# Kernel tuning notes

Measured on AMD Instinct MI355X. Metric: run time of the kernel, lower is better.

The kernel has to match this reference:

```python
import jax, jax.numpy as jnp
import numpy as np

B, S, E, H = 2, 2048, 1024, 16
D = E // H  # head_dim = 64


def setup_inputs() -> dict:
    key = jax.random.key(0)
    ks = jax.random.split(key, 14)
    inp = {
        "query": jax.random.normal(ks[0], (B, S, E), jnp.float32),
        "key": jax.random.normal(ks[1], (B, S, E), jnp.float32),
        "value": jax.random.normal(ks[2], (B, S, E), jnp.float32),
        "adj": jax.random.normal(ks[3], (S, S), jnp.float32),
        "mask": jax.random.randint(ks[4], (B, 1, S, S), 0, 2, jnp.int32),
    }
    sc = 1.0 / np.sqrt(E)
    inp["Wq"] = jax.random.normal(ks[5], (E, E), jnp.float32) * sc
    inp["bq"] = jax.random.normal(ks[6], (E,), jnp.float32) * sc
    inp["Wk"] = jax.random.normal(ks[7], (E, E), jnp.float32) * sc
    inp["bk"] = jax.random.normal(ks[8], (E,), jnp.float32) * sc
    inp["Wv"] = jax.random.normal(ks[9], (E, E), jnp.float32) * sc
    inp["bv"] = jax.random.normal(ks[10], (E,), jnp.float32) * sc
    inp["Wo"] = jax.random.normal(ks[11], (E, E), jnp.float32) * sc
    inp["bo"] = jax.random.normal(ks[12], (E,), jnp.float32) * sc
    return inp


def reference(query, key, value, adj, mask, Wq, bq, Wk, bk, Wv, bv, Wo, bo):
    b, s, _ = query.shape
    # projections, split into heads: [B,S,E] -> [B,H,S,D]
    def heads(x, W, bias):
        y = jnp.einsum("bse,ef->bsf", x, W.T) + bias
        return y.reshape(b, s, H, D).transpose(0, 2, 1, 3)

    Q = heads(query, Wq, bq)
    K = heads(key, Wk, bk)
    V = heads(value, Wv, bv)

    # scores: [B,H,S,S], scaled by sqrt(head_dim), plus adjacency bias
    scores = jnp.einsum("bhqd,bhkd->bhqk", Q, K) / jnp.sqrt(jnp.float32(D))
    scores = scores + adj[None, None, :, :]
    scores = jnp.where(mask == 0, jnp.float32(-jnp.inf), scores)

    weights = jax.nn.softmax(scores, axis=-1)
    out = jnp.einsum("bhqk,bhkd->bhqd", weights, V)
    out = out.transpose(0, 2, 1, 3).reshape(b, s, E)
    return jnp.einsum("bse,ef->bsf", out, Wo.T) + bo
```

## Files before the change

kernel.cpp:

```cpp
#include <hip/hip_runtime.h>


typedef unsigned short ushort_t;
typedef __attribute__((ext_vector_type(8))) short bf16x8;
typedef __attribute__((ext_vector_type(4))) float floatx4;
typedef __attribute__((ext_vector_type(2))) unsigned int uintx2;

#define NB 2
#define NS 2048
#define NE 1024
#define NH 16
#define ND 64
#define LOG2E 1.44269504f

__device__ __forceinline__ unsigned short f2bf(float f) {
  unsigned int u = __float_as_uint(f);
  return (unsigned short)((u + 0x7fffu + ((u >> 16) & 1u)) >> 16);
}
__device__ __forceinline__ float bf2f(unsigned short h) {
  return __uint_as_float(((unsigned int)h) << 16);
}

__device__ __forceinline__ void gload_lds16(const void* g, void* l) {
  __builtin_amdgcn_global_load_lds(
      (const __attribute__((address_space(1))) unsigned int*)g,
      (__attribute__((address_space(3))) unsigned int*)l, 16, 0, 0);
}

__device__ __forceinline__ float fexp2(float x) {
#if __has_builtin(__builtin_amdgcn_exp2f)
  return __builtin_amdgcn_exp2f(x);
#else
  return exp2f(x);
#endif
}

__device__ __forceinline__ unsigned int cvtpk_bf16(float lo, float hi) {
  unsigned int r;
  asm("v_cvt_pk_bf16_f32 %0, %1, %2" : "=v"(r) : "v"(lo), "v"(hi));
  return r;
}

__device__ __forceinline__ void pl32swap(unsigned int& a, unsigned int& b) {
#if __has_builtin(__builtin_amdgcn_permlane32_swap)
  uintx2 r = __builtin_amdgcn_permlane32_swap(a, b, false, false);
  a = r[0]; b = r[1];
#else
  asm("v_permlane32_swap_b32 %0, %1" : "+v"(a), "+v"(b));
#endif
}
__device__ __forceinline__ void pl16swap(unsigned int& a, unsigned int& b) {
#if __has_builtin(__builtin_amdgcn_permlane16_swap)
  uintx2 r = __builtin_amdgcn_permlane16_swap(a, b, false, false);
  a = r[0]; b = r[1];
#else
  asm("v_permlane16_swap_b32 %0, %1" : "+v"(a), "+v"(b));
#endif
}

__global__ __launch_bounds__(256) void convert_kernel(
    const float* __restrict__ q, const float* __restrict__ k, const float* __restrict__ v,
    const float* __restrict__ wq, const float* __restrict__ wk,
    const float* __restrict__ wv, const float* __restrict__ wo,
    const float* __restrict__ adj, const int* __restrict__ mask,
    ushort_t* __restrict__ qb, ushort_t* __restrict__ kb, ushort_t* __restrict__ vb,
    ushort_t* __restrict__ wqb, ushort_t* __restrict__ wkb,
    ushort_t* __restrict__ wvb, ushort_t* __restrict__ wob,
    ushort_t* __restrict__ bias)
{
  const long U1 = (long)NB * NS * NE / 8;
  const long U2 = (long)NE * NE / 8;
  long idx = (long)blockIdx.x * 256 + threadIdx.x;
  const float* src;
  ushort_t* dst;
  if (idx < U1) { src = q; dst = qb; }
  else if ((idx -= U1) < U1) { src = k; dst = kb; }
  else if ((idx -= U1) < U1) { src = v; dst = vb; }
  else if ((idx -= U1) < U2) { src = wq; dst = wqb; }
  else if ((idx -= U2) < U2) { src = wk; dst = wkb; }
  else if ((idx -= U2) < U2) { src = wv; dst = wvb; }
  else if ((idx -= U2) < U2) { src = wo; dst = wob; }
  else {
    idx -= U2;
    long flat = idx * 8;
    long rem = flat & ((1L << 22) - 1);
    const float4* a4 = (const float4*)(adj + rem);
    const int4* m4 = (const int4*)(mask + flat);
    float4 a0 = a4[0], a1 = a4[1];
    int4 m0 = m4[0], m1 = m4[1];
    const float NEGV = -1e30f;
    union { ushort_t us[8]; uint4 v4; } o;
    o.us[0] = f2bf((m0.x ? a0.x : NEGV) * LOG2E);
    o.us[1] = f2bf((m0.y ? a0.y : NEGV) * LOG2E);
    o.us[2] = f2bf((m0.z ? a0.z : NEGV) * LOG2E);
    o.us[3] = f2bf((m0.w ? a0.w : NEGV) * LOG2E);
    o.us[4] = f2bf((m1.x ? a1.x : NEGV) * LOG2E);
    o.us[5] = f2bf((m1.y ? a1.y : NEGV) * LOG2E);
    o.us[6] = f2bf((m1.z ? a1.z : NEGV) * LOG2E);
    o.us[7] = f2bf((m1.w ? a1.w : NEGV) * LOG2E);
    ((uint4*)bias)[idx] = o.v4;
    return;
  }
  const float4* s4 = (const float4*)src;
  float4 a0 = s4[idx * 2], a1 = s4[idx * 2 + 1];
  union { ushort_t us[8]; uint4 v4; } o;
  o.us[0] = f2bf(a0.x); o.us[1] = f2bf(a0.y); o.us[2] = f2bf(a0.z); o.us[3] = f2bf(a0.w);
  o.us[4] = f2bf(a1.x); o.us[5] = f2bf(a1.y); o.us[6] = f2bf(a1.z); o.us[7] = f2bf(a1.w);
  ((uint4*)dst)[idx] = o.v4;
}

__global__ __launch_bounds__(256) void qkv_kernel(
    const ushort_t* __restrict__ xq, const ushort_t* __restrict__ xk, const ushort_t* __restrict__ xv,
    const ushort_t* __restrict__ wqb, const ushort_t* __restrict__ wkb, const ushort_t* __restrict__ wvb,
    const float* __restrict__ bq, const float* __restrict__ bk, const float* __restrict__ bvv,
    ushort_t* __restrict__ Qh, ushort_t* __restrict__ Kh, ushort_t* __restrict__ Vt)
{
  __shared__ __align__(16) ushort_t As[128 * 32];
  __shared__ __align__(16) ushort_t Bs[128 * 32];

  int z = blockIdx.z;
  const ushort_t* X = (z == 0) ? xq : (z == 1) ? xk : xv;
  const ushort_t* W = (z == 0) ? wqb : (z == 1) ? wkb : wvb;
  const float* bias = (z == 0) ? bq : (z == 1) ? bk : bvv;

  int t = threadIdx.x;
  int lane = t & 63, w = t >> 6;
  int quad = lane >> 4, l16 = lane & 15;
  int wr = w >> 1, wc = w & 1;
  int m0 = blockIdx.y * 128, f0 = blockIdx.x * 128;

  floatx4 acc[4][4] = {};

  int arow = t >> 2, apart = t & 3;
  const ushort_t* Xg = X + (long)(m0 + arow) * NE + apart * 8;
  const ushort_t* Wg = W + (long)(f0 + arow) * NE + apart * 8;
  ushort_t* As_t = As + t * 8;
  ushort_t* Bs_t = Bs + t * 8;

  for (int k0 = 0; k0 < NE; k0 += 32) {
    __syncthreads();
    gload_lds16(Xg + k0, As_t);
    gload_lds16(Xg + k0 + 64 * NE, As_t + 64 * 32);
    gload_lds16(Wg + k0, Bs_t);
    gload_lds16(Wg + k0 + 64 * NE, Bs_t + 64 * 32);
    __syncthreads();
    bf16x8 af[4], bf[4];
#pragma unroll
    for (int i = 0; i < 4; i++)
      af[i] = *(const bf16x8*)(As + (wr * 64 + i * 16 + l16) * 32 + quad * 8);
#pragma unroll
    for (int j = 0; j < 4; j++)
      bf[j] = *(const bf16x8*)(Bs + (wc * 64 + j * 16 + l16) * 32 + quad * 8);
#pragma unroll
    for (int i = 0; i < 4; i++)
#pragma unroll
      for (int j = 0; j < 4; j++)
        acc[i][j] = __builtin_amdgcn_mfma_f32_16x16x32_bf16(af[i], bf[j], acc[i][j], 0, 0, 0);
  }

  ushort_t* Out = (z == 0) ? Qh : (z == 1) ? Kh : Vt;
  bool isV = (z == 2);
#pragma unroll
  for (int j = 0; j < 4; j++) {
    int f = f0 + wc * 64 + j * 16 + l16;
    float bval = bias[f];
    int h = f >> 6, d = f & 63;
#pragma unroll
    for (int i = 0; i < 4; i++) {
      int mbase = m0 + wr * 64 + i * 16 + quad * 4;
#pragma unroll
      for (int r = 0; r < 4; r++) {
        int m = mbase + r;
        int b = m >> 11, s = m & 2047;
        float y = acc[i][j][r] + bval;
        long off;
        if (!isV) off = ((long)(b * NH + h) * NS + s) * ND + d;
        else      off = ((long)(b * NH + h) * ND + d) * NS + s;
        Out[off] = f2bf(y);
      }
    }
  }
}

__global__ __launch_bounds__(256, 2) void attn_kernel(
    const ushort_t* __restrict__ Qh, const ushort_t* __restrict__ Kh,
    const ushort_t* __restrict__ Vt, const ushort_t* __restrict__ bias,
    ushort_t* __restrict__ aout)
{
  __shared__ __align__(16) ushort_t Qs[128 * 64];
  __shared__ __align__(16) ushort_t Ks[2][32 * 64];
  __shared__ __align__(16) ushort_t Vts[2][64 * 32];

  int t = threadIdx.x, lane = t & 63, w = t >> 6;
  int quad = lane >> 4, l16 = lane & 15;
  int orig = blockIdx.y * 16 + blockIdx.x;
  int wg = ((orig & 7) << 6) | (orig >> 3);
  int qt = wg & 15, bh = wg >> 4;
  int bb = bh >> 4, h = bh & 15;
  int q0 = qt * 128;

  const ushort_t* Qg = Qh + ((long)bh * NS + q0) * ND;
#pragma unroll
  for (int c = 0; c < 4; c++) {
    int idx = c * 256 + t;
    gload_lds16(Qg + (long)(idx >> 3) * ND + (idx & 7) * 8, Qs + idx * 8);
  }

  const ushort_t* Kg = Kh + (long)bh * NS * ND;
  const ushort_t* Vg = Vt + (long)bh * ND * NS;
  int krow = t >> 3;
  int kc = (t & 7) ^ (krow & 7);
  int vsr = t >> 3;
  int vc = (t & 7) ^ (vsr & 7);
  int vrow = vsr * 2 + (vc >> 2);
  int vpart = vc & 3;
  const ushort_t* Kgp = Kg + (long)krow * ND + kc * 8;
  const ushort_t* Vgp = Vg + (long)vrow * NS + vpart * 8;

  gload_lds16(Kgp, &Ks[0][t * 8]);
  gload_lds16(Vgp, &Vts[0][t * 8]);

  const ushort_t* bg0 = bias + (long)bb * NS * NS
                      + (long)(q0 + w * 32 + l16) * NS + quad * 4;
  const ushort_t* bg1 = bg0 + 16 * NS;
  uintx2 bc[2][2];
  bc[0][0] = *(const uintx2*)bg0;
  bc[0][1] = *(const uintx2*)(bg0 + 16);
  bc[1][0] = *(const uintx2*)bg1;
  bc[1][1] = *(const uintx2*)(bg1 + 16);

  __syncthreads();

  bf16x8 aq[2][2];
#pragma unroll
  for (int m = 0; m < 2; m++)
#pragma unroll
    for (int kd = 0; kd < 2; kd++)
      aq[m][kd] = *(const bf16x8*)(Qs + (w * 32 + m * 16 + l16) * 64 + kd * 32 + quad * 8);

  floatx4 acc[2][4] = {};
  float lsum[2] = {0.f, 0.f};

  const int ks_x = l16 & 7;
  const int vs_c = (((l16 & 1) * 4 + quad) ^ (l16 >> 1)) * 8;

#pragma unroll 2
  for (int kt = 0; kt < NS / 32; kt++) {
    int cur = kt & 1;
    __syncthreads();
    if (kt < NS / 32 - 1) {
      gload_lds16(Kgp + (long)(kt + 1) * (32 * ND), &Ks[cur ^ 1][t * 8]);
      gload_lds16(Vgp + (kt + 1) * 32, &Vts[cur ^ 1][t * 8]);
    }
    uintx2 bn[2][2];
#pragma unroll
    for (int m = 0; m < 2; m++) { bn[m][0] = bc[m][0]; bn[m][1] = bc[m][1]; }
    if (kt < NS / 32 - 1) {
      bn[0][0] = *(const uintx2*)(bg0 + (kt + 1) * 32);
      bn[0][1] = *(const uintx2*)(bg0 + (kt + 1) * 32 + 16);
      bn[1][0] = *(const uintx2*)(bg1 + (kt + 1) * 32);
      bn[1][1] = *(const uintx2*)(bg1 + (kt + 1) * 32 + 16);
    }

    const ushort_t* Kb = Ks[cur];
    const ushort_t* Vb = Vts[cur];
    bf16x8 bk[2][2], bv[4];
#pragma unroll
    for (int jk = 0; jk < 2; jk++)
#pragma unroll
      for (int kd = 0; kd < 2; kd++)
        bk[jk][kd] = *(const bf16x8*)(Kb + (jk * 16 + l16) * 64
                                         + ((kd * 4 + quad) ^ ks_x) * 8);
#pragma unroll
    for (int j = 0; j < 4; j++)
      bv[j] = *(const bf16x8*)(Vb + (j * 8 + (l16 >> 1)) * 64 + vs_c);

#pragma unroll
    for (int m = 0; m < 2; m++) {
      floatx4 sc[2] = {};
#pragma unroll
      for (int jk = 0; jk < 2; jk++)
#pragma unroll
        for (int kd = 0; kd < 2; kd++)
          sc[jk] = __builtin_amdgcn_mfma_f32_16x16x32_bf16(bk[jk][kd], aq[m][kd], sc[jk], 0, 0, 0);

      float p[2][4];
#pragma unroll
      for (int jk = 0; jk < 2; jk++) {
        unsigned int d0 = bc[m][jk][0], d1 = bc[m][jk][1];
        float b0 = __uint_as_float(d0 << 16);
        float b1 = __uint_as_float(d0 & 0xffff0000u);
        float b2 = __uint_as_float(d1 << 16);
        float b3 = __uint_as_float(d1 & 0xffff0000u);
        p[jk][0] = fexp2(fmaf(sc[jk][0], 0.125f * LOG2E, b0));
        p[jk][1] = fexp2(fmaf(sc[jk][1], 0.125f * LOG2E, b1));
        p[jk][2] = fexp2(fmaf(sc[jk][2], 0.125f * LOG2E, b2));
        p[jk][3] = fexp2(fmaf(sc[jk][3], 0.125f * LOG2E, b3));
      }
      lsum[m] += ((p[0][0] + p[0][1]) + (p[0][2] + p[0][3]))
               + ((p[1][0] + p[1][1]) + (p[1][2] + p[1][3]));

      unsigned int A0 = cvtpk_bf16(p[0][0], p[0][1]);
      unsigned int A1 = cvtpk_bf16(p[0][2], p[0][3]);
      unsigned int B0 = cvtpk_bf16(p[1][0], p[1][1]);
      unsigned int B1 = cvtpk_bf16(p[1][2], p[1][3]);
      pl32swap(A0, B0); pl16swap(A0, B0);
      pl32swap(A1, B1); pl16swap(A1, B1);
      union { unsigned int u[4]; bf16x8 v8; } pf;
      pf.u[0] = A0; pf.u[1] = A1; pf.u[2] = B0; pf.u[3] = B1;
#pragma unroll
      for (int j = 0; j < 4; j++)
        acc[m][j] = __builtin_amdgcn_mfma_f32_16x16x32_bf16(pf.v8, bv[j], acc[m][j], 0, 0, 0);
    }
#pragma unroll
    for (int m = 0; m < 2; m++) { bc[m][0] = bn[m][0]; bc[m][1] = bn[m][1]; }
  }

#pragma unroll
  for (int m = 0; m < 2; m++) {
    float s = lsum[m];
    s += __shfl_xor(s, 16);
    s += __shfl_xor(s, 32);
    lsum[m] = s;
  }

  ushort_t* og = aout + (long)bb * NS * NE + h * ND;
#pragma unroll
  for (int m = 0; m < 2; m++)
#pragma unroll
    for (int r = 0; r < 4; r++) {
      float inv = 1.0f / __shfl(lsum[m], quad * 4 + r);
      int qg = q0 + w * 32 + m * 16 + quad * 4 + r;
#pragma unroll
      for (int j = 0; j < 4; j++)
        og[(long)qg * NE + j * 16 + l16] = f2bf(acc[m][j][r] * inv);
    }
}

__global__ __launch_bounds__(256) void oproj_kernel(
    const ushort_t* __restrict__ A, const ushort_t* __restrict__ Wob,
    const float* __restrict__ bo, float* __restrict__ out)
{
  __shared__ __align__(16) ushort_t As[128 * 32];
  __shared__ __align__(16) ushort_t Bs[64 * 32];

  int t = threadIdx.x;
  int lane = t & 63, w = t >> 6;
  int quad = lane >> 4, l16 = lane & 15;
  int wr = w >> 1, wc = w & 1;
  int m0 = blockIdx.y * 128, f0 = blockIdx.x * 64;

  floatx4 acc[4][2] = {};
  int arow = t >> 2, apart = t & 3;
  const ushort_t* Xg = A + (long)(m0 + arow) * NE + apart * 8;
  const ushort_t* Wg = Wob + (long)(f0 + arow) * NE + apart * 8;
  ushort_t* As_t = As + t * 8;
  ushort_t* Bs_t = Bs + t * 8;
  bool bstage = (arow < 64);

  for (int k0 = 0; k0 < NE; k0 += 32) {
    __syncthreads();
    gload_lds16(Xg + k0, As_t);
    gload_lds16(Xg + k0 + 64 * NE, As_t + 64 * 32);
    if (bstage) gload_lds16(Wg + k0, Bs_t);
    __syncthreads();
    bf16x8 af[4], bf[2];
#pragma unroll
    for (int i = 0; i < 4; i++)
      af[i] = *(const bf16x8*)(As + (wr * 64 + i * 16 + l16) * 32 + quad * 8);
#pragma unroll
    for (int j = 0; j < 2; j++)
      bf[j] = *(const bf16x8*)(Bs + (wc * 32 + j * 16 + l16) * 32 + quad * 8);
#pragma unroll
    for (int i = 0; i < 4; i++)
#pragma unroll
      for (int j = 0; j < 2; j++)
        acc[i][j] = __builtin_amdgcn_mfma_f32_16x16x32_bf16(af[i], bf[j], acc[i][j], 0, 0, 0);
  }

#pragma unroll
  for (int j = 0; j < 2; j++) {
    int f = f0 + wc * 32 + j * 16 + l16;
    float bval = bo[f];
#pragma unroll
    for (int i = 0; i < 4; i++) {
      int mbase = m0 + wr * 64 + i * 16 + quad * 4;
#pragma unroll
      for (int r = 0; r < 4; r++) {
        int m = mbase + r;
        out[(long)m * NE + f] = acc[i][j][r] + bval;
      }
    }
  }
}

extern "C" void kernel_launch(void* const* d_in, const int* in_sizes, int n_in,
                              void* d_out, int out_size, void* d_ws, size_t ws_size,
                              hipStream_t stream) {
  const float* query = (const float*)d_in[0];
  const float* key   = (const float*)d_in[1];
  const float* value = (const float*)d_in[2];
  const float* adj   = (const float*)d_in[3];
  const int*   mask  = (const int*)d_in[4];
  const float* Wq = (const float*)d_in[5];
  const float* bq = (const float*)d_in[6];
  const float* Wk = (const float*)d_in[7];
  const float* bk = (const float*)d_in[8];
  const float* Wv = (const float*)d_in[9];
  const float* bv = (const float*)d_in[10];
  const float* Wo = (const float*)d_in[11];
  const float* bo = (const float*)d_in[12];
  float* out = (float*)d_out;

  char* ws = (char*)d_ws;
  const size_t MB = 1ull << 20;
  ushort_t* qb   = (ushort_t*)(ws + 0 * MB);
  ushort_t* kb   = (ushort_t*)(ws + 8 * MB);
  ushort_t* vb   = (ushort_t*)(ws + 16 * MB);
  ushort_t* wqb  = (ushort_t*)(ws + 24 * MB);
  ushort_t* wkb  = (ushort_t*)(ws + 26 * MB);
  ushort_t* wvb  = (ushort_t*)(ws + 28 * MB);
  ushort_t* wob  = (ushort_t*)(ws + 30 * MB);
  ushort_t* Qh   = (ushort_t*)(ws + 32 * MB);
  ushort_t* Kh   = (ushort_t*)(ws + 40 * MB);
  ushort_t* Vt   = (ushort_t*)(ws + 48 * MB);
  ushort_t* aout = (ushort_t*)(ws + 56 * MB);
  ushort_t* bias = (ushort_t*)(ws + 64 * MB);

  convert_kernel<<<12288, 256, 0, stream>>>(query, key, value, Wq, Wk, Wv, Wo,
                                            adj, mask, qb, kb, vb, wqb, wkb, wvb, wob, bias);
  qkv_kernel<<<dim3(8, 32, 3), 256, 0, stream>>>(qb, kb, vb, wqb, wkb, wvb,
                                                 bq, bk, bv, Qh, Kh, Vt);
  attn_kernel<<<dim3(16, 32), 256, 0, stream>>>(Qh, Kh, Vt, bias, aout);
  oproj_kernel<<<dim3(16, 32), 256, 0, stream>>>(aout, wob, bo, out);
}
```

Before: 313.3 us.

## Triple-buffer GEMM loads and split attention keys across two waves per block

The QKV and output-projection GEMMs move to a three-stage LDS ring with explicit vmcnt waits and a single barrier per iteration, so global loads can overlap MFMA work. The attention kernel is restructured into 128-thread blocks of 64 queries. Each of its two waves handles half of the key range with its own private K/V double buffer and no block barriers inside the loop. The two partial outputs and row sums are then merged through LDS. This adds more register pressure (4x4 accumulators), hand-tuned waitcnt counts that could break correctness if they are wrong, and a reduction epilogue.

New measurement: 328.7 us. +4.9%, slower.

```diff
diff --git a/kernel.cpp b/kernel.cpp
--- a/kernel.cpp
+++ b/kernel.cpp
@@ -25,6 +25,13 @@
   __builtin_amdgcn_global_load_lds(
       (const __attribute__((address_space(1))) unsigned int*)g,
       (__attribute__((address_space(3))) unsigned int*)l, 16, 0, 0);
+}
+
+__device__ __forceinline__ uintx2 gload8(const void* p) {
+  uintx2 r;
+  asm volatile("global_load_dwordx2 %0, %1, off"
+               : "=v"(r) : "v"(p) : "memory");
+  return r;
 }
 
 __device__ __forceinline__ float fexp2(float x) {
@@ -115,8 +122,8 @@
     const float* __restrict__ bq, const float* __restrict__ bk, const float* __restrict__ bvv,
     ushort_t* __restrict__ Qh, ushort_t* __restrict__ Kh, ushort_t* __restrict__ Vt)
 {
-  __shared__ __align__(16) ushort_t As[128 * 32];
-  __shared__ __align__(16) ushort_t Bs[128 * 32];
+  __shared__ __align__(16) ushort_t As[3][128 * 32];
+  __shared__ __align__(16) ushort_t Bs[3][128 * 32];
 
   int z = blockIdx.z;
   const ushort_t* X = (z == 0) ? xq : (z == 1) ? xk : xv;
@@ -129,34 +136,45 @@
   int wr = w >> 1, wc = w & 1;
   int m0 = blockIdx.y * 128, f0 = blockIdx.x * 128;
 
-  floatx4 acc[4][4] = {};
-
   int arow = t >> 2, apart = t & 3;
   const ushort_t* Xg = X + (long)(m0 + arow) * NE + apart * 8;
   const ushort_t* Wg = W + (long)(f0 + arow) * NE + apart * 8;
-  ushort_t* As_t = As + t * 8;
-  ushort_t* Bs_t = Bs + t * 8;
-
-  for (int k0 = 0; k0 < NE; k0 += 32) {
-    __syncthreads();
-    gload_lds16(Xg + k0, As_t);
-    gload_lds16(Xg + k0 + 64 * NE, As_t + 64 * 32);
-    gload_lds16(Wg + k0, Bs_t);
-    gload_lds16(Wg + k0 + 64 * NE, Bs_t + 64 * 32);
-    __syncthreads();
+
+  auto STAGE = [&](int kk, int buf) {
+    int k0 = kk * 32;
+    gload_lds16(Xg + k0, &As[buf][t * 8]);
+    gload_lds16(Xg + k0 + 64 * NE, &As[buf][64 * 32 + t * 8]);
+    gload_lds16(Wg + k0, &Bs[buf][t * 8]);
+    gload_lds16(Wg + k0 + 64 * NE, &Bs[buf][64 * 32 + t * 8]);
+  };
+  STAGE(0, 0);
+  STAGE(1, 1);
+
+  floatx4 acc[4][4] = {};
+  int b = 0;
+  for (int k = 0; k < 32; ++k) {
+    asm volatile("s_waitcnt vmcnt(4) lgkmcnt(0)" ::: "memory");
+    __builtin_amdgcn_s_barrier();
+    __builtin_amdgcn_sched_barrier(0);
+    int nb = (b == 0) ? 2 : b - 1;
+    STAGE((k + 2) & 31, nb);
+    const ushort_t* Ab = As[b];
+    const ushort_t* Bb = Bs[b];
     bf16x8 af[4], bf[4];
 #pragma unroll
     for (int i = 0; i < 4; i++)
-      af[i] = *(const bf16x8*)(As + (wr * 64 + i * 16 + l16) * 32 + quad * 8);
-#pragma unroll
-    for (int j = 0; j < 4; j++)
-      bf[j] = *(const bf16x8*)(Bs + (wc * 64 + j * 16 + l16) * 32 + quad * 8);
+      af[i] = *(const bf16x8*)(Ab + (wr * 64 + i * 16 + l16) * 32 + quad * 8);
+#pragma unroll
+    for (int j = 0; j < 4; j++)
+      bf[j] = *(const bf16x8*)(Bb + (wc * 64 + j * 16 + l16) * 32 + quad * 8);
 #pragma unroll
     for (int i = 0; i < 4; i++)
 #pragma unroll
       for (int j = 0; j < 4; j++)
         acc[i][j] = __builtin_amdgcn_mfma_f32_16x16x32_bf16(af[i], bf[j], acc[i][j], 0, 0, 0);
-  }
+    b = (b == 2) ? 0 : b + 1;
+  }
+  asm volatile("s_waitcnt vmcnt(0)" ::: "memory");
 
   ushort_t* Out = (z == 0) ? Qh : (z == 1) ? Kh : Vt;
   bool isV = (z == 2);
@@ -171,99 +189,99 @@
 #pragma unroll
       for (int r = 0; r < 4; r++) {
         int m = mbase + r;
-        int b = m >> 11, s = m & 2047;
+        int bb2 = m >> 11, s = m & 2047;
         float y = acc[i][j][r] + bval;
         long off;
-        if (!isV) off = ((long)(b * NH + h) * NS + s) * ND + d;
-        else      off = ((long)(b * NH + h) * ND + d) * NS + s;
+        if (!isV) off = ((long)(bb2 * NH + h) * NS + s) * ND + d;
+        else      off = ((long)(bb2 * NH + h) * ND + d) * NS + s;
         Out[off] = f2bf(y);
       }
     }
   }
 }
 
-__global__ __launch_bounds__(256, 2) void attn_kernel(
+__global__ __launch_bounds__(128, 2) void attn_kernel(
     const ushort_t* __restrict__ Qh, const ushort_t* __restrict__ Kh,
     const ushort_t* __restrict__ Vt, const ushort_t* __restrict__ bias,
     ushort_t* __restrict__ aout)
 {
-  __shared__ __align__(16) ushort_t Qs[128 * 64];
-  __shared__ __align__(16) ushort_t Ks[2][32 * 64];
-  __shared__ __align__(16) ushort_t Vts[2][64 * 32];
+  __shared__ __align__(16) ushort_t KVs[2][2][4096];
+  __shared__ float Ls[2][64];
 
   int t = threadIdx.x, lane = t & 63, w = t >> 6;
   int quad = lane >> 4, l16 = lane & 15;
-  int orig = blockIdx.y * 16 + blockIdx.x;
-  int wg = ((orig & 7) << 6) | (orig >> 3);
-  int qt = wg & 15, bh = wg >> 4;
+  int orig = blockIdx.x;
+  int wg = ((orig & 7) << 7) | (orig >> 3);
+  int qt = wg & 31, bh = wg >> 5;
   int bb = bh >> 4, h = bh & 15;
-  int q0 = qt * 128;
+  int q0 = qt * 64;
+  int kbase = w * (NS / 2);
 
   const ushort_t* Qg = Qh + ((long)bh * NS + q0) * ND;
-#pragma unroll
-  for (int c = 0; c < 4; c++) {
-    int idx = c * 256 + t;
-    gload_lds16(Qg + (long)(idx >> 3) * ND + (idx & 7) * 8, Qs + idx * 8);
-  }
-
   const ushort_t* Kg = Kh + (long)bh * NS * ND;
   const ushort_t* Vg = Vt + (long)bh * ND * NS;
-  int krow = t >> 3;
-  int kc = (t & 7) ^ (krow & 7);
-  int vsr = t >> 3;
-  int vc = (t & 7) ^ (vsr & 7);
-  int vrow = vsr * 2 + (vc >> 2);
-  int vpart = vc & 3;
-  const ushort_t* Kgp = Kg + (long)krow * ND + kc * 8;
-  const ushort_t* Vgp = Vg + (long)vrow * NS + vpart * 8;
-
-  gload_lds16(Kgp, &Ks[0][t * 8]);
-  gload_lds16(Vgp, &Vts[0][t * 8]);
-
-  const ushort_t* bg0 = bias + (long)bb * NS * NS
-                      + (long)(q0 + w * 32 + l16) * NS + quad * 4;
-  const ushort_t* bg1 = bg0 + 16 * NS;
-  uintx2 bc[2][2];
-  bc[0][0] = *(const uintx2*)bg0;
-  bc[0][1] = *(const uintx2*)(bg0 + 16);
-  bc[1][0] = *(const uintx2*)bg1;
-  bc[1][1] = *(const uintx2*)(bg1 + 16);
-
-  __syncthreads();
-
-  bf16x8 aq[2][2];
-#pragma unroll
-  for (int m = 0; m < 2; m++)
+  const ushort_t* biasg = bias + (long)bb * NS * NS;
+
+  bf16x8 aq[4][2];
+#pragma unroll
+  for (int m = 0; m < 4; m++)
 #pragma unroll
     for (int kd = 0; kd < 2; kd++)
-      aq[m][kd] = *(const bf16x8*)(Qs + (w * 32 + m * 16 + l16) * 64 + kd * 32 + quad * 8);
-
-  floatx4 acc[2][4] = {};
-  float lsum[2] = {0.f, 0.f};
-
+      aq[m][kd] = *(const bf16x8*)(Qg + (long)(m * 16 + l16) * ND + kd * 32 + quad * 8);
+
+  const ushort_t* pK[4];
+  const ushort_t* pV[4];
+#pragma unroll
+  for (int j = 0; j < 4; j++) {
+    int ci = j * 64 + lane;
+    int row = ci >> 3, cc = (ci & 7) ^ (row & 7);
+    pK[j] = Kg + (long)row * ND + cc * 8;
+    int sr = ci >> 3, vc2 = (ci & 7) ^ (sr & 7);
+    int vrow = sr * 2 + (vc2 >> 2), vpart = vc2 & 3;
+    pV[j] = Vg + (long)vrow * NS + vpart * 8;
+  }
+  const ushort_t* pB[4];
+#pragma unroll
+  for (int m = 0; m < 4; m++)
+    pB[m] = biasg + (long)(q0 + m * 16 + l16) * NS + quad * 4;
+
+  auto STAGE = [&](int tile, int buf) {
+    int k0 = kbase + tile * 32;
+    ushort_t* Kb = &KVs[w][buf][0];
+    ushort_t* Vb = &KVs[w][buf][2048];
+#pragma unroll
+    for (int j = 0; j < 4; j++)
+      gload_lds16(pK[j] + (long)k0 * ND, Kb + (j * 64 + lane) * 8);
+#pragma unroll
+    for (int j = 0; j < 4; j++)
+      gload_lds16(pV[j] + k0, Vb + (j * 64 + lane) * 8);
+  };
+
+  uintx2 bc[4][2], bn[4][2];
+  auto BLOAD = [&](uintx2 (&dst)[4][2], int tile) {
+    int k0 = kbase + tile * 32;
+#pragma unroll
+    for (int m = 0; m < 4; m++) {
+      dst[m][0] = gload8(pB[m] + k0);
+      dst[m][1] = gload8(pB[m] + k0 + 16);
+    }
+  };
+
+  STAGE(0, 0);
+  BLOAD(bc, 0);
+  STAGE(1, 1);
+
+  floatx4 acc[4][4] = {};
+  float lsum[4] = {0.f, 0.f, 0.f, 0.f};
   const int ks_x = l16 & 7;
   const int vs_c = (((l16 & 1) * 4 + quad) ^ (l16 >> 1)) * 8;
 
 #pragma unroll 2
-  for (int kt = 0; kt < NS / 32; kt++) {
-    int cur = kt & 1;
-    __syncthreads();
-    if (kt < NS / 32 - 1) {
-      gload_lds16(Kgp + (long)(kt + 1) * (32 * ND), &Ks[cur ^ 1][t * 8]);
-      gload_lds16(Vgp + (kt + 1) * 32, &Vts[cur ^ 1][t * 8]);
-    }
-    uintx2 bn[2][2];
-#pragma unroll
-    for (int m = 0; m < 2; m++) { bn[m][0] = bc[m][0]; bn[m][1] = bc[m][1]; }
-    if (kt < NS / 32 - 1) {
-      bn[0][0] = *(const uintx2*)(bg0 + (kt + 1) * 32);
-      bn[0][1] = *(const uintx2*)(bg0 + (kt + 1) * 32 + 16);
-      bn[1][0] = *(const uintx2*)(bg1 + (kt + 1) * 32);
-      bn[1][1] = *(const uintx2*)(bg1 + (kt + 1) * 32 + 16);
-    }
-
-    const ushort_t* Kb = Ks[cur];
-    const ushort_t* Vb = Vts[cur];
+  for (int i = 0; i < 32; ++i) {
+    int cur = i & 1;
+    const ushort_t* Kb = &KVs[w][cur][0];
+    const ushort_t* Vb = &KVs[w][cur][2048];
+    asm volatile("s_waitcnt vmcnt(16)" ::: "memory");
     bf16x8 bk[2][2], bv[4];
 #pragma unroll
     for (int jk = 0; jk < 2; jk++)
@@ -274,9 +292,14 @@
 #pragma unroll
     for (int j = 0; j < 4; j++)
       bv[j] = *(const bf16x8*)(Vb + (j * 8 + (l16 >> 1)) * 64 + vs_c);
-
-#pragma unroll
-    for (int m = 0; m < 2; m++) {
+    asm volatile("s_waitcnt lgkmcnt(0)" ::: "memory");
+    BLOAD(bn, (i + 1) & 31);
+    STAGE((i + 2) & 31, cur);
+    asm volatile("s_waitcnt vmcnt(24)" ::: "memory");
+    __builtin_amdgcn_sched_barrier(0);
+
+#pragma unroll
+    for (int m = 0; m < 4; m++) {
       floatx4 sc[2] = {};
 #pragma unroll
       for (int jk = 0; jk < 2; jk++)
@@ -313,36 +336,60 @@
         acc[m][j] = __builtin_amdgcn_mfma_f32_16x16x32_bf16(pf.v8, bv[j], acc[m][j], 0, 0, 0);
     }
 #pragma unroll
-    for (int m = 0; m < 2; m++) { bc[m][0] = bn[m][0]; bc[m][1] = bn[m][1]; }
-  }
-
-#pragma unroll
-  for (int m = 0; m < 2; m++) {
+    for (int m = 0; m < 4; m++) { bc[m][0] = bn[m][0]; bc[m][1] = bn[m][1]; }
+  }
+  asm volatile("s_waitcnt vmcnt(0)" ::: "memory");
+
+#pragma unroll
+  for (int m = 0; m < 4; m++) {
     float s = lsum[m];
     s += __shfl_xor(s, 16);
     s += __shfl_xor(s, 32);
     lsum[m] = s;
   }
 
+  __syncthreads();
+  float* C = (float*)&KVs[0][0][0];
+  int mo0 = (1 - w) * 2;
+#pragma unroll
+  for (int mm = 0; mm < 2; mm++) {
+    int m = mo0 + mm;
+#pragma unroll
+    for (int j = 0; j < 4; j++)
+      *(floatx4*)(C + (j * 16 + l16) * 64 + (((m * 4 + quad) ^ l16) * 4)) = acc[m][j];
+  }
+  if (lane < 16) {
+    Ls[w][mo0 * 16 + lane]      = lsum[mo0];
+    Ls[w][mo0 * 16 + 16 + lane] = lsum[mo0 + 1];
+  }
+  __syncthreads();
+
+  int ms = w * 2;
   ushort_t* og = aout + (long)bb * NS * NE + h * ND;
 #pragma unroll
-  for (int m = 0; m < 2; m++)
+  for (int mm = 0; mm < 2; mm++) {
+    int m = ms + mm;
+#pragma unroll
+    for (int j = 0; j < 4; j++)
+      acc[m][j] += *(const floatx4*)(C + (j * 16 + l16) * 64 + (((m * 4 + quad) ^ l16) * 4));
+    float lt = lsum[m] + Ls[1 - w][m * 16 + l16];
 #pragma unroll
     for (int r = 0; r < 4; r++) {
-      float inv = 1.0f / __shfl(lsum[m], quad * 4 + r);
-      int qg = q0 + w * 32 + m * 16 + quad * 4 + r;
+      float inv = 1.0f / __shfl(lt, quad * 4 + r);
+      int qg = q0 + m * 16 + quad * 4 + r;
 #pragma unroll
       for (int j = 0; j < 4; j++)
         og[(long)qg * NE + j * 16 + l16] = f2bf(acc[m][j][r] * inv);
     }
+  }
 }
 
 __global__ __launch_bounds__(256) void oproj_kernel(
     const ushort_t* __restrict__ A, const ushort_t* __restrict__ Wob,
     const float* __restrict__ bo, float* __restrict__ out)
 {
-  __shared__ __align__(16) ushort_t As[128 * 32];
-  __shared__ __align__(16) ushort_t Bs[64 * 32];
+  __shared__ __align__(16) ushort_t As[3][128 * 32];
+  __shared__ __align__(16) ushort_t Bs[3][64 * 32];
 
   int t = threadIdx.x;
   int lane = t & 63, w = t >> 6;
@@ -350,33 +397,44 @@
   int wr = w >> 1, wc = w & 1;
   int m0 = blockIdx.y * 128, f0 = blockIdx.x * 64;
 
-  floatx4 acc[4][2] = {};
   int arow = t >> 2, apart = t & 3;
   const ushort_t* Xg = A + (long)(m0 + arow) * NE + apart * 8;
   const ushort_t* Wg = Wob + (long)(f0 + arow) * NE + apart * 8;
-  ushort_t* As_t = As + t * 8;
-  ushort_t* Bs_t = Bs + t * 8;
-  bool bstage = (arow < 64);
-
-  for (int k0 = 0; k0 < NE; k0 += 32) {
-    __syncthreads();
-    gload_lds16(Xg + k0, As_t);
-    gload_lds16(Xg + k0 + 64 * NE, As_t + 64 * 32);
-    if (bstage) gload_lds16(Wg + k0, Bs_t);
-    __syncthreads();
+
+  auto STAGE = [&](int kk, int buf) {
+    int k0 = kk * 32;
+    gload_lds16(Xg + k0, &As[buf][t * 8]);
+    gload_lds16(Xg + k0 + 64 * NE, &As[buf][64 * 32 + t * 8]);
+    gload_lds16(Wg + k0, &Bs[buf][t * 8]);
+  };
+  STAGE(0, 0);
+  STAGE(1, 1);
+
+  floatx4 acc[4][2] = {};
+  int b = 0;
+  for (int k = 0; k < 32; ++k) {
+    asm volatile("s_waitcnt vmcnt(3) lgkmcnt(0)" ::: "memory");
+    __builtin_amdgcn_s_barrier();
+    __builtin_amdgcn_sched_barrier(0);
+    int nb = (b == 0) ? 2 : b - 1;
+    STAGE((k + 2) & 31, nb);
+    const ushort_t* Ab = As[b];
+    const ushort_t* Bb = Bs[b];
     bf16x8 af[4], bf[2];
 #pragma unroll
     for (int i = 0; i < 4; i++)
-      af[i] = *(const bf16x8*)(As + (wr * 64 + i * 16 + l16) * 32 + quad * 8);
+      af[i] = *(const bf16x8*)(Ab + (wr * 64 + i * 16 + l16) * 32 + quad * 8);
 #pragma unroll
     for (int j = 0; j < 2; j++)
-      bf[j] = *(const bf16x8*)(Bs + (wc * 32 + j * 16 + l16) * 32 + quad * 8);
+      bf[j] = *(const bf16x8*)(Bb + (wc * 32 + j * 16 + l16) * 32 + quad * 8);
 #pragma unroll
     for (int i = 0; i < 4; i++)
 #pragma unroll
       for (int j = 0; j < 2; j++)
         acc[i][j] = __builtin_amdgcn_mfma_f32_16x16x32_bf16(af[i], bf[j], acc[i][j], 0, 0, 0);
-  }
+    b = (b == 2) ? 0 : b + 1;
+  }
+  asm volatile("s_waitcnt vmcnt(0)" ::: "memory");
 
 #pragma unroll
   for (int j = 0; j < 2; j++) {
@@ -431,6 +489,6 @@
                                             adj, mask, qb, kb, vb, wqb, wkb, wvb, wob, bias);
   qkv_kernel<<<dim3(8, 32, 3), 256, 0, stream>>>(qb, kb, vb, wqb, wkb, wvb,
                                                  bq, bk, bv, Qh, Kh, Vt);
-  attn_kernel<<<dim3(16, 32), 256, 0, stream>>>(Qh, Kh, Vt, bias, aout);
+  attn_kernel<<<dim3(1024), 128, 0, stream>>>(Qh, Kh, Vt, bias, aout);
   oproj_kernel<<<dim3(16, 32), 256, 0, stream>>>(aout, wob, bo, out);
 }
```
